# Optimization experiments

Hardware: AMD Instinct MI355X
Metric: run time of the kernel (lower is better)

## Reference

```python
import jax, jax.numpy as jnp
import numpy as np

N_VISIBLE = 50000
N_HIDDEN = 5000
N_NODES = N_VISIBLE + N_HIDDEN
N_EDGES = 1_000_000
BATCH = 128


def setup_inputs() -> dict:
    key = jax.random.key(0)
    k1, k2, k3, k4, k5 = jax.random.split(key, 5)
    # parameters, initialized as in the torch module
    linear = 0.05 * (2.0 * jax.random.uniform(k1, (N_NODES,), dtype=jnp.float32) - 1.0)
    quadratic = 5.0 * (2.0 * jax.random.uniform(k2, (N_EDGES,), dtype=jnp.float32) - 1.0)
    # bipartite visible-hidden edges -> CSR-like flat buffers (via segment ids)
    flat_adj = jax.random.randint(k3, (N_EDGES,), 0, N_VISIBLE, dtype=jnp.int32).astype(jnp.int64)  # visible endpoint per edge
    seg_ids = jax.random.randint(k4, (N_EDGES,), 0, N_HIDDEN, dtype=jnp.int32).astype(jnp.int64)    # hidden bin per edge
    flat_j_idx = jnp.arange(N_EDGES, dtype=jnp.int64)  # quadratic coefficient index per flat entry
    hidden_idx = jnp.arange(N_HIDDEN, dtype=jnp.int64) + N_VISIBLE
    # observed spin configurations in {0,1} (mapped to +-1 inside reference)
    s = jax.random.randint(k5, (BATCH, N_NODES), 0, 2, dtype=jnp.int32)
    return {
        "linear": linear,
        "quadratic": quadratic,
        "s": s,
        "flat_adj": flat_adj,
        "flat_j_idx": flat_j_idx,
        "seg_ids": seg_ids,
        "hidden_idx": hidden_idx,
        "n_hidden": N_HIDDEN,
    }


def reference(linear, quadratic, s, flat_adj, flat_j_idx, seg_ids, hidden_idx, n_hidden):
    """Per-hidden-unit effective field + conditional spin expectation.

    eff[b, k] = linear[hidden_idx[k]]
                + sum_{e : seg_ids[e]==k} quadratic[flat_j_idx[e]] * s_pm[b, flat_adj[e]]
    returns tanh(-eff)  (conditional expectation of hidden spins given visibles)
    """
    s_pm = (2 * s - 1).astype(linear.dtype)                 # {0,1} -> {-1,+1}, (B, N)
    w = quadratic[flat_j_idx]                               # (E,)
    contrib = s_pm[:, flat_adj].T * w[:, None]              # (E, B) gathered neighbor terms
    field = jax.ops.segment_sum(contrib, seg_ids, num_segments=n_hidden)  # (K, B)
    eff = field.T + linear[hidden_idx][None, :]             # (B, K)
    return jnp.tanh(-eff)
```

## Files before the change

kernel.cpp:

```cpp
#include <hip/hip_runtime.h>
#include <math.h>
#include <stdint.h>

#define NV 50000
#define NH 5000
#define NN 55000
#define NCB 313
#define BCAP 4096
#define KSLOT 384
#define CHUNK 4096


__device__ __forceinline__ uint32_t selmask(uint32_t word, uint32_t bsh) {
#if __has_builtin(__builtin_amdgcn_sbfe)
    return (uint32_t)__builtin_amdgcn_sbfe((int)word, bsh, 1u);
#else
    return (uint32_t)((int32_t)(word << (31u - bsh)) >> 31);
#endif
}

__global__ void __launch_bounds__(256) pack_zero_kernel(
        const int* __restrict__ s, uint32_t* __restrict__ bits,
        uint32_t* __restrict__ coarse_cnt) {
    if (blockIdx.x == 0)
        for (int i = threadIdx.x; i < NCB; i += 256) coarse_cnt[i] = 0u;
    int tid = blockIdx.x * 256 + threadIdx.x;
    int v = tid >> 2;
    int g = tid & 3;
    if (v >= NV) return;
    const int* col = s + (size_t)g * 32 * NN + v;
    uint32_t w = 0;
#pragma unroll
    for (int j = 0; j < 32; ++j)
        w |= (uint32_t)(col[(size_t)j * NN] & 1) << j;
    bits[(size_t)v * 4 + g] = w;
}

__global__ void __launch_bounds__(256) coarse_split_kernel(
        const int4* __restrict__ seg4, const int4* __restrict__ adj4,
        const float4* __restrict__ quad4,
        uint32_t* __restrict__ coarse_cnt, uint2* __restrict__ recs, int E) {
    __shared__ uint32_t hist[320];
    __shared__ uint32_t loc[320];
    __shared__ uint32_t cur[NCB];
    __shared__ uint32_t gbase[NCB];
    __shared__ __align__(16) uint2 st[CHUNK];
    __shared__ uint32_t dst[CHUNK];
    const int tid = threadIdx.x;
    for (int i = tid; i < 320; i += 256) hist[i] = 0u;
    __syncthreads();

    const int c0 = blockIdx.x * CHUNK;
    const int nloc = min(CHUNK, E - c0);
    int kreg[16];
#pragma unroll
    for (int j = 0; j < 4; ++j) {
        int t4 = (c0 >> 2) + j * 256 + tid;
        bool ok = t4 < ((c0 + nloc) >> 2);
        int4 sg = ok ? seg4[t4] : make_int4(-1, -1, -1, -1);
        kreg[j * 4 + 0] = sg.x; kreg[j * 4 + 1] = sg.y;
        kreg[j * 4 + 2] = sg.z; kreg[j * 4 + 3] = sg.w;
        if (ok) {
            atomicAdd(&hist[sg.x >> 4], 1u);
            atomicAdd(&hist[sg.y >> 4], 1u);
            atomicAdd(&hist[sg.z >> 4], 1u);
            atomicAdd(&hist[sg.w >> 4], 1u);
        }
    }
    __syncthreads();
    for (int i = tid; i < NCB; i += 256)
        gbase[i] = atomicAdd(&coarse_cnt[i], hist[i]);
    for (int i = tid; i < 320; i += 256) loc[i] = hist[i];
    __syncthreads();
    for (int d = 1; d < 320; d <<= 1) {
        uint32_t v0 = 0, v1 = 0;
        int i1 = tid + 256;
        if (tid >= d) v0 = loc[tid - d];
        if (i1 < 320 && i1 >= d) v1 = loc[i1 - d];
        __syncthreads();
        if (tid >= d) loc[tid] += v0;
        if (i1 < 320 && i1 >= d) loc[i1] += v1;
        __syncthreads();
    }
    for (int i = tid; i < NCB; i += 256) cur[i] = loc[i] - hist[i];
    __syncthreads();
#pragma unroll
    for (int j = 0; j < 4; ++j) {
        int t4 = (c0 >> 2) + j * 256 + tid;
        if (t4 < ((c0 + nloc) >> 2)) {
            int4 a = adj4[t4];
            float4 q = quad4[t4];
#pragma unroll
            for (int cmp = 0; cmp < 4; ++cmp) {
                int k = kreg[j * 4 + cmp];
                int v = (cmp == 0) ? a.x : (cmp == 1) ? a.y : (cmp == 2) ? a.z : a.w;
                float w = (cmp == 0) ? q.x : (cmp == 1) ? q.y : (cmp == 2) ? q.z : q.w;
                int bk = k >> 4;
                uint32_t slot = atomicAdd(&cur[bk], 1u);
                uint32_t rank = gbase[bk] + (slot - (loc[bk] - hist[bk]));
                st[slot] = make_uint2((uint32_t)v | ((uint32_t)(k & 15) << 16),
                                      __float_as_uint(w));
                dst[slot] = (rank < BCAP) ? (uint32_t)bk * BCAP + rank : ~0u;
            }
        }
    }
    __syncthreads();
    for (int i = tid; i < nloc; i += 256) {
        uint32_t d = dst[i];
        if (d != ~0u) recs[d] = st[i];
    }
}

__global__ void __launch_bounds__(256) quarter_field_kernel(
        const uint32_t* __restrict__ coarse_cnt, const uint2* __restrict__ recs,
        const uint4* __restrict__ bits4, const float* __restrict__ linear,
        float* __restrict__ out) {
    const int x = blockIdx.x;
    const int j = (x & 7) * 157 + (x >> 3);
    const int bkt = j >> 2;
    const int q = j & 3;
    if (bkt >= NCB) return;
    const int tid = threadIdx.x;

    __shared__ uint32_t cur4[4];
    __shared__ float swp[4];
    __shared__ __align__(16) uint2 st4[4][KSLOT];
    __shared__ __align__(16) uint32_t rows[2][5][KSLOT];
    __shared__ float part[2][256];

    if (tid < 4) cur4[tid] = 0u;
    __syncthreads();

    int cnt = (int)min(coarse_cnt[bkt], (uint32_t)BCAP);
    const uint2* region = recs + (size_t)bkt * BCAP;
    for (int i = tid; i < cnt; i += 256) {
        uint2 r = region[i];
        int kl = (int)((r.x >> 16) & 15u);
        if ((kl >> 2) == q) {
            uint32_t p = atomicAdd(&cur4[kl & 3], 1u);
            if (p < KSLOT) st4[kl & 3][p] = r;
        }
    }
    __syncthreads();

    const int b = tid & 127;
    const int grp = tid >> 7;
    const uint32_t bsh = (uint32_t)(b & 31);
    const int widx = b >> 5;

    for (int rnd = 0; rnd < 2; ++rnd) {
        int kl = rnd * 2 + grp;
        int c = min((int)cur4[kl], KSLOT);
        int T8 = (c + 7) & ~7;
        float sw = 0.f;
        for (int t = c + b; t < T8; t += 128) rows[grp][4][t] = 0u;
        for (int t = b; t < c; t += 128) {
            uint2 r = st4[kl][t];
            uint4 mw = bits4[r.x & 0xFFFFu];
            rows[grp][0][t] = mw.x;
            rows[grp][1][t] = mw.y;
            rows[grp][2][t] = mw.z;
            rows[grp][3][t] = mw.w;
            rows[grp][4][t] = r.y;
            sw += __uint_as_float(r.y);
        }
#pragma unroll
        for (int off = 32; off; off >>= 1) sw += __shfl_down(sw, off);
        if ((tid & 63) == 0) swp[tid >> 6] = sw;
        __syncthreads();

#pragma unroll
        for (int kk = 0; kk < 2; ++kk) {
            int T8k = (min((int)cur4[rnd * 2 + kk], KSLOT) + 7) & ~7;
            const uint32_t* mrow = rows[kk][widx];
            const uint32_t* wrow = rows[kk][4];
            float a0 = 0.f, a1 = 0.f, a2 = 0.f, a3 = 0.f;
            for (int i = grp * 4; i < T8k; i += 8) {
                uint4 mm = *(const uint4*)(mrow + i);
                uint4 ww = *(const uint4*)(wrow + i);
                a0 += __uint_as_float(ww.x & selmask(mm.x, bsh));
                a1 += __uint_as_float(ww.y & selmask(mm.y, bsh));
                a2 += __uint_as_float(ww.z & selmask(mm.z, bsh));
                a3 += __uint_as_float(ww.w & selmask(mm.w, bsh));
            }
            part[kk][tid] = (a0 + a1) + (a2 + a3);
        }
        __syncthreads();
        if (tid < 128) {
            int k0 = bkt * 16 + q * 4 + rnd * 2;
            if (k0 + 1 < NH) {
                float acc0 = part[0][tid] + part[0][tid + 128];
                float acc1 = part[1][tid] + part[1][tid + 128];
                float e0 = 2.f * acc0 - (swp[0] + swp[1]) + linear[NV + k0];
                float e1 = 2.f * acc1 - (swp[2] + swp[3]) + linear[NV + k0 + 1];
                float2 o = make_float2(tanhf(-e0), tanhf(-e1));
                *(float2*)(out + (size_t)tid * NH + k0) = o;
            }
        }
        __syncthreads();
    }
}

extern "C" void kernel_launch(void* const* d_in, const int* in_sizes, int n_in,
                              void* d_out, int out_size, void* d_ws, size_t ws_size,
                              hipStream_t stream) {
    const float* linear = (const float*)d_in[0];
    const float* quad   = (const float*)d_in[1];
    const int*   s      = (const int*)d_in[2];
    const int*   adj    = (const int*)d_in[3];
    const int*   seg    = (const int*)d_in[5];
    const int E = in_sizes[5];
    float* out = (float*)d_out;

    char* ws = (char*)d_ws;
    uint32_t* bits       = (uint32_t*)(ws);
    uint32_t* coarse_cnt = (uint32_t*)(ws + 800000);
    uint2*    recs       = (uint2*)   (ws + 801280);

    pack_zero_kernel<<<(NV * 4 + 255) / 256, 256, 0, stream>>>(s, bits, coarse_cnt);
    const int nchunk = (E + CHUNK - 1) / CHUNK;
    coarse_split_kernel<<<nchunk, 256, 0, stream>>>(
        (const int4*)seg, (const int4*)adj, (const float4*)quad, coarse_cnt, recs, E);
    quarter_field_kernel<<<1256, 256, 0, stream>>>(coarse_cnt, recs, (const uint4*)bits,
                                                   linear, out);
}
```

Before: 134.2 us.

## Use finer 4-unit buckets with direct scatter and fused gather in field kernel

The edge split now bins edges into 1250 buckets of 4 hidden units instead of 313 buckets of 16. Records are scattered straight to global memory rather than staged in shared memory for a coalesced write-out, and the block-wide prefix scan is gone. The field kernel now handles one bucket per block and gathers the bitmask rows directly while scanning the region. This drops the old scheme where four blocks each re-read and filtered a 16-unit region. The costs are less coalesced global scatter writes, a larger record buffer, and reading each region twice, once per round.

```diff
diff --git a/kernel.cpp b/kernel.cpp
--- a/kernel.cpp
+++ b/kernel.cpp
@@ -5,8 +5,9 @@
 #define NV 50000
 #define NH 5000
 #define NN 55000
-#define NCB 313
-#define BCAP 4096
+#define NCB 1250
+#define NCBP 1280
+#define BCAP 1280
 #define KSLOT 384
 #define CHUNK 4096
 
@@ -36,58 +37,45 @@
     bits[(size_t)v * 4 + g] = w;
 }
 
-__global__ void __launch_bounds__(256) coarse_split_kernel(
+__global__ void __launch_bounds__(256) split_kernel(
         const int4* __restrict__ seg4, const int4* __restrict__ adj4,
         const float4* __restrict__ quad4,
         uint32_t* __restrict__ coarse_cnt, uint2* __restrict__ recs, int E) {
-    __shared__ uint32_t hist[320];
-    __shared__ uint32_t loc[320];
-    __shared__ uint32_t cur[NCB];
-    __shared__ uint32_t gbase[NCB];
-    __shared__ __align__(16) uint2 st[CHUNK];
-    __shared__ uint32_t dst[CHUNK];
+    __shared__ uint32_t hist[NCBP];
+    __shared__ uint32_t curb[NCBP];
+    __shared__ uint32_t gbase[NCBP];
     const int tid = threadIdx.x;
-    for (int i = tid; i < 320; i += 256) hist[i] = 0u;
+    for (int i = tid; i < NCBP; i += 256) { hist[i] = 0u; curb[i] = 0u; }
     __syncthreads();
 
     const int c0 = blockIdx.x * CHUNK;
     const int nloc = min(CHUNK, E - c0);
+    const int t4max = (c0 + nloc) >> 2;
     int kreg[16];
 #pragma unroll
     for (int j = 0; j < 4; ++j) {
         int t4 = (c0 >> 2) + j * 256 + tid;
-        bool ok = t4 < ((c0 + nloc) >> 2);
+        bool ok = t4 < t4max;
         int4 sg = ok ? seg4[t4] : make_int4(-1, -1, -1, -1);
         kreg[j * 4 + 0] = sg.x; kreg[j * 4 + 1] = sg.y;
         kreg[j * 4 + 2] = sg.z; kreg[j * 4 + 3] = sg.w;
         if (ok) {
-            atomicAdd(&hist[sg.x >> 4], 1u);
-            atomicAdd(&hist[sg.y >> 4], 1u);
-            atomicAdd(&hist[sg.z >> 4], 1u);
-            atomicAdd(&hist[sg.w >> 4], 1u);
+            atomicAdd(&hist[sg.x >> 2], 1u);
+            atomicAdd(&hist[sg.y >> 2], 1u);
+            atomicAdd(&hist[sg.z >> 2], 1u);
+            atomicAdd(&hist[sg.w >> 2], 1u);
         }
     }
     __syncthreads();
-    for (int i = tid; i < NCB; i += 256)
-        gbase[i] = atomicAdd(&coarse_cnt[i], hist[i]);
-    for (int i = tid; i < 320; i += 256) loc[i] = hist[i];
-    __syncthreads();
-    for (int d = 1; d < 320; d <<= 1) {
-        uint32_t v0 = 0, v1 = 0;
-        int i1 = tid + 256;
-        if (tid >= d) v0 = loc[tid - d];
-        if (i1 < 320 && i1 >= d) v1 = loc[i1 - d];
-        __syncthreads();
-        if (tid >= d) loc[tid] += v0;
-        if (i1 < 320 && i1 >= d) loc[i1] += v1;
-        __syncthreads();
-    }
-    for (int i = tid; i < NCB; i += 256) cur[i] = loc[i] - hist[i];
+    for (int i = tid; i < NCB; i += 256) {
+        uint32_t h = hist[i];
+        if (h) gbase[i] = atomicAdd(&coarse_cnt[i], h);
+    }
     __syncthreads();
 #pragma unroll
     for (int j = 0; j < 4; ++j) {
         int t4 = (c0 >> 2) + j * 256 + tid;
-        if (t4 < ((c0 + nloc) >> 2)) {
+        if (t4 < t4max) {
             int4 a = adj4[t4];
             float4 q = quad4[t4];
 #pragma unroll
@@ -95,83 +83,84 @@
                 int k = kreg[j * 4 + cmp];
                 int v = (cmp == 0) ? a.x : (cmp == 1) ? a.y : (cmp == 2) ? a.z : a.w;
                 float w = (cmp == 0) ? q.x : (cmp == 1) ? q.y : (cmp == 2) ? q.z : q.w;
-                int bk = k >> 4;
-                uint32_t slot = atomicAdd(&cur[bk], 1u);
-                uint32_t rank = gbase[bk] + (slot - (loc[bk] - hist[bk]));
-                st[slot] = make_uint2((uint32_t)v | ((uint32_t)(k & 15) << 16),
-                                      __float_as_uint(w));
-                dst[slot] = (rank < BCAP) ? (uint32_t)bk * BCAP + rank : ~0u;
+                int bk = k >> 2;
+                uint32_t rank = atomicAdd(&curb[bk], 1u);
+                uint32_t pos = gbase[bk] + rank;
+                if (pos < BCAP)
+                    recs[(size_t)bk * BCAP + pos] =
+                        make_uint2((uint32_t)v | ((uint32_t)(k & 3) << 16),
+                                   __float_as_uint(w));
             }
         }
     }
-    __syncthreads();
-    for (int i = tid; i < nloc; i += 256) {
-        uint32_t d = dst[i];
-        if (d != ~0u) recs[d] = st[i];
-    }
-}
-
-__global__ void __launch_bounds__(256) quarter_field_kernel(
+}
+
+__global__ void __launch_bounds__(256, 8) field_kernel(
         const uint32_t* __restrict__ coarse_cnt, const uint2* __restrict__ recs,
         const uint4* __restrict__ bits4, const float* __restrict__ linear,
         float* __restrict__ out) {
     const int x = blockIdx.x;
-    const int j = (x & 7) * 157 + (x >> 3);
-    const int bkt = j >> 2;
-    const int q = j & 3;
+    const int bkt = (x & 7) * 157 + (x >> 3);
     if (bkt >= NCB) return;
     const int tid = threadIdx.x;
 
-    __shared__ uint32_t cur4[4];
-    __shared__ float swp[4];
-    __shared__ __align__(16) uint2 st4[4][KSLOT];
+    __shared__ uint32_t cur2[2];
+    __shared__ float swp[4][2];
     __shared__ __align__(16) uint32_t rows[2][5][KSLOT];
     __shared__ float part[2][256];
 
-    if (tid < 4) cur4[tid] = 0u;
-    __syncthreads();
-
-    int cnt = (int)min(coarse_cnt[bkt], (uint32_t)BCAP);
-    const uint2* region = recs + (size_t)bkt * BCAP;
-    for (int i = tid; i < cnt; i += 256) {
-        uint2 r = region[i];
-        int kl = (int)((r.x >> 16) & 15u);
-        if ((kl >> 2) == q) {
-            uint32_t p = atomicAdd(&cur4[kl & 3], 1u);
-            if (p < KSLOT) st4[kl & 3][p] = r;
-        }
-    }
-    __syncthreads();
+    const int cnt = (int)min(coarse_cnt[bkt], (uint32_t)BCAP);
+    const uint2* __restrict__ region = recs + (size_t)bkt * BCAP;
 
     const int b = tid & 127;
     const int grp = tid >> 7;
     const uint32_t bsh = (uint32_t)(b & 31);
     const int widx = b >> 5;
+    const int lane = tid & 63;
+    const int wid = tid >> 6;
 
     for (int rnd = 0; rnd < 2; ++rnd) {
-        int kl = rnd * 2 + grp;
-        int c = min((int)cur4[kl], KSLOT);
-        int T8 = (c + 7) & ~7;
-        float sw = 0.f;
-        for (int t = c + b; t < T8; t += 128) rows[grp][4][t] = 0u;
-        for (int t = b; t < c; t += 128) {
-            uint2 r = st4[kl][t];
-            uint4 mw = bits4[r.x & 0xFFFFu];
-            rows[grp][0][t] = mw.x;
-            rows[grp][1][t] = mw.y;
-            rows[grp][2][t] = mw.z;
-            rows[grp][3][t] = mw.w;
-            rows[grp][4][t] = r.y;
-            sw += __uint_as_float(r.y);
-        }
-#pragma unroll
-        for (int off = 32; off; off >>= 1) sw += __shfl_down(sw, off);
-        if ((tid & 63) == 0) swp[tid >> 6] = sw;
+        if (tid < 2) cur2[tid] = 0u;
+        __syncthreads();
+
+        float s0 = 0.f, s1 = 0.f;
+        for (int i = tid; i < cnt; i += 256) {
+            uint2 r = region[i];
+            int kl = (int)((r.x >> 16) & 3u);
+            if ((kl >> 1) == rnd) {
+                int kk = kl & 1;
+                uint32_t p = atomicAdd(&cur2[kk], 1u);
+                if (p < KSLOT) {
+                    uint4 mw = bits4[r.x & 0xFFFFu];
+                    rows[kk][0][p] = mw.x;
+                    rows[kk][1][p] = mw.y;
+                    rows[kk][2][p] = mw.z;
+                    rows[kk][3][p] = mw.w;
+                    rows[kk][4][p] = r.y;
+                    float w = __uint_as_float(r.y);
+                    if (kk == 0) s0 += w; else s1 += w;
+                }
+            }
+        }
+#pragma unroll
+        for (int off = 32; off; off >>= 1) {
+            s0 += __shfl_down(s0, off);
+            s1 += __shfl_down(s1, off);
+        }
+        if (lane == 0) { swp[wid][0] = s0; swp[wid][1] = s1; }
         __syncthreads();
 
 #pragma unroll
         for (int kk = 0; kk < 2; ++kk) {
-            int T8k = (min((int)cur4[rnd * 2 + kk], KSLOT) + 7) & ~7;
+            int c = min((int)cur2[kk], KSLOT);
+            int T8 = (c + 7) & ~7;
+            for (int t = c + tid; t < T8; t += 256) rows[kk][4][t] = 0u;
+        }
+        __syncthreads();
+
+#pragma unroll
+        for (int kk = 0; kk < 2; ++kk) {
+            int T8k = (min((int)cur2[kk], KSLOT) + 7) & ~7;
             const uint32_t* mrow = rows[kk][widx];
             const uint32_t* wrow = rows[kk][4];
             float a0 = 0.f, a1 = 0.f, a2 = 0.f, a3 = 0.f;
@@ -186,16 +175,17 @@
             part[kk][tid] = (a0 + a1) + (a2 + a3);
         }
         __syncthreads();
+
         if (tid < 128) {
-            int k0 = bkt * 16 + q * 4 + rnd * 2;
-            if (k0 + 1 < NH) {
-                float acc0 = part[0][tid] + part[0][tid + 128];
-                float acc1 = part[1][tid] + part[1][tid + 128];
-                float e0 = 2.f * acc0 - (swp[0] + swp[1]) + linear[NV + k0];
-                float e1 = 2.f * acc1 - (swp[2] + swp[3]) + linear[NV + k0 + 1];
-                float2 o = make_float2(tanhf(-e0), tanhf(-e1));
-                *(float2*)(out + (size_t)tid * NH + k0) = o;
-            }
+            int k0 = bkt * 4 + rnd * 2;
+            float acc0 = part[0][tid] + part[0][tid + 128];
+            float acc1 = part[1][tid] + part[1][tid + 128];
+            float sum0 = swp[0][0] + swp[1][0] + swp[2][0] + swp[3][0];
+            float sum1 = swp[0][1] + swp[1][1] + swp[2][1] + swp[3][1];
+            float e0 = 2.f * acc0 - sum0 + linear[NV + k0];
+            float e1 = 2.f * acc1 - sum1 + linear[NV + k0 + 1];
+            float2 o = make_float2(tanhf(-e0), tanhf(-e1));
+            *(float2*)(out + (size_t)tid * NH + k0) = o;
         }
         __syncthreads();
     }
@@ -215,12 +205,12 @@
     char* ws = (char*)d_ws;
     uint32_t* bits       = (uint32_t*)(ws);
     uint32_t* coarse_cnt = (uint32_t*)(ws + 800000);
-    uint2*    recs       = (uint2*)   (ws + 801280);
+    uint2*    recs       = (uint2*)   (ws + 805120);
 
     pack_zero_kernel<<<(NV * 4 + 255) / 256, 256, 0, stream>>>(s, bits, coarse_cnt);
     const int nchunk = (E + CHUNK - 1) / CHUNK;
-    coarse_split_kernel<<<nchunk, 256, 0, stream>>>(
+    split_kernel<<<nchunk, 256, 0, stream>>>(
         (const int4*)seg, (const int4*)adj, (const float4*)quad, coarse_cnt, recs, E);
-    quarter_field_kernel<<<1256, 256, 0, stream>>>(coarse_cnt, recs, (const uint4*)bits,
-                                                   linear, out);
-}
+    field_kernel<<<1256, 256, 0, stream>>>(coarse_cnt, recs, (const uint4*)bits,
+                                           linear, out);
+}
```

After: 134.7 us. About the same (+0.3%).

## Replace two-level coarse bucketing with direct per-hidden-unit global atomic binning

Applied to the files above, without the earlier changes.

The shared-memory histogram, scan and coarse bucket scatter are replaced by a simple split kernel that does one global atomicAdd per edge on a per-hidden-unit counter and writes the record directly into a fixed KSLOT-sized slot region. The field kernel then reads each hidden unit's records straight from global memory, with no re-filtering of a 16-unit coarse bucket, and gets a launch_bounds occupancy hint. This removes the block-level histogram and scan work and the redundant bucket reads in the field kernel. In exchange it issues a million global atomics contending over 5000 counters and scatters 8-byte stores randomly.

```diff
diff --git a/kernel.cpp b/kernel.cpp
--- a/kernel.cpp
+++ b/kernel.cpp
@@ -5,10 +5,8 @@
 #define NV 50000
 #define NH 5000
 #define NN 55000
-#define NCB 313
-#define BCAP 4096
 #define KSLOT 384
-#define CHUNK 4096
+#define NFB 1250
 
 
 __device__ __forceinline__ uint32_t selmask(uint32_t word, uint32_t bsh) {
@@ -21,9 +19,9 @@
 
 __global__ void __launch_bounds__(256) pack_zero_kernel(
         const int* __restrict__ s, uint32_t* __restrict__ bits,
-        uint32_t* __restrict__ coarse_cnt) {
+        uint32_t* __restrict__ cnt) {
     if (blockIdx.x == 0)
-        for (int i = threadIdx.x; i < NCB; i += 256) coarse_cnt[i] = 0u;
+        for (int i = threadIdx.x; i < NH; i += 256) cnt[i] = 0u;
     int tid = blockIdx.x * 256 + threadIdx.x;
     int v = tid >> 2;
     int g = tid & 3;
@@ -36,127 +34,56 @@
     bits[(size_t)v * 4 + g] = w;
 }
 
-__global__ void __launch_bounds__(256) coarse_split_kernel(
+__global__ void __launch_bounds__(256) split_kernel(
         const int4* __restrict__ seg4, const int4* __restrict__ adj4,
         const float4* __restrict__ quad4,
-        uint32_t* __restrict__ coarse_cnt, uint2* __restrict__ recs, int E) {
-    __shared__ uint32_t hist[320];
-    __shared__ uint32_t loc[320];
-    __shared__ uint32_t cur[NCB];
-    __shared__ uint32_t gbase[NCB];
-    __shared__ __align__(16) uint2 st[CHUNK];
-    __shared__ uint32_t dst[CHUNK];
-    const int tid = threadIdx.x;
-    for (int i = tid; i < 320; i += 256) hist[i] = 0u;
-    __syncthreads();
-
-    const int c0 = blockIdx.x * CHUNK;
-    const int nloc = min(CHUNK, E - c0);
-    int kreg[16];
+        uint32_t* __restrict__ cnt, uint2* __restrict__ recs, int E) {
+    int t4 = blockIdx.x * 256 + threadIdx.x;
+    if (t4 >= (E >> 2)) return;
+    int4 sg = seg4[t4];
+    int4 a  = adj4[t4];
+    float4 q = quad4[t4];
 #pragma unroll
-    for (int j = 0; j < 4; ++j) {
-        int t4 = (c0 >> 2) + j * 256 + tid;
-        bool ok = t4 < ((c0 + nloc) >> 2);
-        int4 sg = ok ? seg4[t4] : make_int4(-1, -1, -1, -1);
-        kreg[j * 4 + 0] = sg.x; kreg[j * 4 + 1] = sg.y;
-        kreg[j * 4 + 2] = sg.z; kreg[j * 4 + 3] = sg.w;
-        if (ok) {
-            atomicAdd(&hist[sg.x >> 4], 1u);
-            atomicAdd(&hist[sg.y >> 4], 1u);
-            atomicAdd(&hist[sg.z >> 4], 1u);
-            atomicAdd(&hist[sg.w >> 4], 1u);
-        }
-    }
-    __syncthreads();
-    for (int i = tid; i < NCB; i += 256)
-        gbase[i] = atomicAdd(&coarse_cnt[i], hist[i]);
-    for (int i = tid; i < 320; i += 256) loc[i] = hist[i];
-    __syncthreads();
-    for (int d = 1; d < 320; d <<= 1) {
-        uint32_t v0 = 0, v1 = 0;
-        int i1 = tid + 256;
-        if (tid >= d) v0 = loc[tid - d];
-        if (i1 < 320 && i1 >= d) v1 = loc[i1 - d];
-        __syncthreads();
-        if (tid >= d) loc[tid] += v0;
-        if (i1 < 320 && i1 >= d) loc[i1] += v1;
-        __syncthreads();
-    }
-    for (int i = tid; i < NCB; i += 256) cur[i] = loc[i] - hist[i];
-    __syncthreads();
-#pragma unroll
-    for (int j = 0; j < 4; ++j) {
-        int t4 = (c0 >> 2) + j * 256 + tid;
-        if (t4 < ((c0 + nloc) >> 2)) {
-            int4 a = adj4[t4];
-            float4 q = quad4[t4];
-#pragma unroll
-            for (int cmp = 0; cmp < 4; ++cmp) {
-                int k = kreg[j * 4 + cmp];
-                int v = (cmp == 0) ? a.x : (cmp == 1) ? a.y : (cmp == 2) ? a.z : a.w;
-                float w = (cmp == 0) ? q.x : (cmp == 1) ? q.y : (cmp == 2) ? q.z : q.w;
-                int bk = k >> 4;
-                uint32_t slot = atomicAdd(&cur[bk], 1u);
-                uint32_t rank = gbase[bk] + (slot - (loc[bk] - hist[bk]));
-                st[slot] = make_uint2((uint32_t)v | ((uint32_t)(k & 15) << 16),
-                                      __float_as_uint(w));
-                dst[slot] = (rank < BCAP) ? (uint32_t)bk * BCAP + rank : ~0u;
-            }
-        }
-    }
-    __syncthreads();
-    for (int i = tid; i < nloc; i += 256) {
-        uint32_t d = dst[i];
-        if (d != ~0u) recs[d] = st[i];
+    for (int cmp = 0; cmp < 4; ++cmp) {
+        int k = (cmp == 0) ? sg.x : (cmp == 1) ? sg.y : (cmp == 2) ? sg.z : sg.w;
+        int v = (cmp == 0) ? a.x  : (cmp == 1) ? a.y  : (cmp == 2) ? a.z  : a.w;
+        float w = (cmp == 0) ? q.x : (cmp == 1) ? q.y : (cmp == 2) ? q.z : q.w;
+        uint32_t slot = atomicAdd(&cnt[k], 1u);
+        if (slot < KSLOT)
+            recs[(size_t)k * KSLOT + slot] =
+                make_uint2((uint32_t)v, __float_as_uint(w));
     }
 }
 
-__global__ void __launch_bounds__(256) quarter_field_kernel(
-        const uint32_t* __restrict__ coarse_cnt, const uint2* __restrict__ recs,
+__global__ void __launch_bounds__(256, 8) field_kernel(
+        const uint32_t* __restrict__ cnt, const uint2* __restrict__ recs,
         const uint4* __restrict__ bits4, const float* __restrict__ linear,
         float* __restrict__ out) {
     const int x = blockIdx.x;
-    const int j = (x & 7) * 157 + (x >> 3);
-    const int bkt = j >> 2;
-    const int q = j & 3;
-    if (bkt >= NCB) return;
+    const int blk = (x & 7) * 157 + (x >> 3);
+    if (blk >= NFB) return;
     const int tid = threadIdx.x;
 
-    __shared__ uint32_t cur4[4];
     __shared__ float swp[4];
-    __shared__ __align__(16) uint2 st4[4][KSLOT];
+    __shared__ int ccnt[2];
     __shared__ __align__(16) uint32_t rows[2][5][KSLOT];
     __shared__ float part[2][256];
-
-    if (tid < 4) cur4[tid] = 0u;
-    __syncthreads();
-
-    int cnt = (int)min(coarse_cnt[bkt], (uint32_t)BCAP);
-    const uint2* region = recs + (size_t)bkt * BCAP;
-    for (int i = tid; i < cnt; i += 256) {
-        uint2 r = region[i];
-        int kl = (int)((r.x >> 16) & 15u);
-        if ((kl >> 2) == q) {
-            uint32_t p = atomicAdd(&cur4[kl & 3], 1u);
-            if (p < KSLOT) st4[kl & 3][p] = r;
-        }
-    }
-    __syncthreads();
 
     const int b = tid & 127;
     const int grp = tid >> 7;
     const uint32_t bsh = (uint32_t)(b & 31);
     const int widx = b >> 5;
+    const int lane = tid & 63;
+    const int wid = tid >> 6;
 
     for (int rnd = 0; rnd < 2; ++rnd) {
-        int kl = rnd * 2 + grp;
-        int c = min((int)cur4[kl], KSLOT);
-        int T8 = (c + 7) & ~7;
+        const int k = blk * 4 + rnd * 2 + grp;
+        const int c = min((int)cnt[k], KSLOT);
+        const uint2* __restrict__ reg = recs + (size_t)k * KSLOT;
         float sw = 0.f;
-        for (int t = c + b; t < T8; t += 128) rows[grp][4][t] = 0u;
         for (int t = b; t < c; t += 128) {
-            uint2 r = st4[kl][t];
-            uint4 mw = bits4[r.x & 0xFFFFu];
+            uint2 r = reg[t];
+            uint4 mw = bits4[r.x];
             rows[grp][0][t] = mw.x;
             rows[grp][1][t] = mw.y;
             rows[grp][2][t] = mw.z;
@@ -164,14 +91,17 @@
             rows[grp][4][t] = r.y;
             sw += __uint_as_float(r.y);
         }
+        const int T8 = (c + 7) & ~7;
+        for (int t = c + b; t < T8; t += 128) rows[grp][4][t] = 0u;
+        if (b == 0) ccnt[grp] = c;
 #pragma unroll
         for (int off = 32; off; off >>= 1) sw += __shfl_down(sw, off);
-        if ((tid & 63) == 0) swp[tid >> 6] = sw;
+        if (lane == 0) swp[wid] = sw;
         __syncthreads();
 
 #pragma unroll
         for (int kk = 0; kk < 2; ++kk) {
-            int T8k = (min((int)cur4[rnd * 2 + kk], KSLOT) + 7) & ~7;
+            const int T8k = (ccnt[kk] + 7) & ~7;
             const uint32_t* mrow = rows[kk][widx];
             const uint32_t* wrow = rows[kk][4];
             float a0 = 0.f, a1 = 0.f, a2 = 0.f, a3 = 0.f;
@@ -186,16 +116,15 @@
             part[kk][tid] = (a0 + a1) + (a2 + a3);
         }
         __syncthreads();
+
         if (tid < 128) {
-            int k0 = bkt * 16 + q * 4 + rnd * 2;
-            if (k0 + 1 < NH) {
-                float acc0 = part[0][tid] + part[0][tid + 128];
-                float acc1 = part[1][tid] + part[1][tid + 128];
-                float e0 = 2.f * acc0 - (swp[0] + swp[1]) + linear[NV + k0];
-                float e1 = 2.f * acc1 - (swp[2] + swp[3]) + linear[NV + k0 + 1];
-                float2 o = make_float2(tanhf(-e0), tanhf(-e1));
-                *(float2*)(out + (size_t)tid * NH + k0) = o;
-            }
+            int k0 = blk * 4 + rnd * 2;
+            float acc0 = part[0][tid] + part[0][tid + 128];
+            float acc1 = part[1][tid] + part[1][tid + 128];
+            float e0 = 2.f * acc0 - (swp[0] + swp[1]) + linear[NV + k0];
+            float e1 = 2.f * acc1 - (swp[2] + swp[3]) + linear[NV + k0 + 1];
+            float2 o = make_float2(tanhf(-e0), tanhf(-e1));
+            *(float2*)(out + (size_t)tid * NH + k0) = o;
         }
         __syncthreads();
     }
@@ -213,14 +142,13 @@
     float* out = (float*)d_out;
 
     char* ws = (char*)d_ws;
-    uint32_t* bits       = (uint32_t*)(ws);
-    uint32_t* coarse_cnt = (uint32_t*)(ws + 800000);
-    uint2*    recs       = (uint2*)   (ws + 801280);
+    uint32_t* bits = (uint32_t*)(ws);
+    uint32_t* cnt  = (uint32_t*)(ws + 800000);
+    uint2*    recs = (uint2*)   (ws + 820480);
 
-    pack_zero_kernel<<<(NV * 4 + 255) / 256, 256, 0, stream>>>(s, bits, coarse_cnt);
-    const int nchunk = (E + CHUNK - 1) / CHUNK;
-    coarse_split_kernel<<<nchunk, 256, 0, stream>>>(
-        (const int4*)seg, (const int4*)adj, (const float4*)quad, coarse_cnt, recs, E);
-    quarter_field_kernel<<<1256, 256, 0, stream>>>(coarse_cnt, recs, (const uint4*)bits,
-                                                   linear, out);
+    pack_zero_kernel<<<(NV * 4 + 255) / 256, 256, 0, stream>>>(s, bits, cnt);
+    split_kernel<<<((E >> 2) + 255) / 256, 256, 0, stream>>>(
+        (const int4*)seg, (const int4*)adj, (const float4*)quad, cnt, recs, E);
+    field_kernel<<<1256, 256, 0, stream>>>(cnt, recs, (const uint4*)bits,
+                                           linear, out);
 }
```

After: 176.9 us. 1.32x slower.
